# Kernel tuning notes

Hardware: AMD Instinct MI355X
Metric: run time of the kernel (lower is better)

Reference implementation:

```python
import jax, jax.numpy as jnp
import numpy as np

N_A = 50000
N_B = 50000
E = 500000
D = 128


def setup_inputs() -> dict:
    key = jax.random.key(0)
    ks = jax.random.split(key, 16)
    s = 0.02
    inp = {
        "x_a": jax.random.normal(ks[0], (N_A, D), jnp.float32),
        "x_b": jax.random.normal(ks[1], (N_B, D), jnp.float32),
        # shared GraphEdgeWeight params
        "Wp": jax.random.normal(ks[2], (D, D), jnp.float32) * s,
        "bp": jnp.zeros((D,), jnp.float32),
        "Wc": jax.random.normal(ks[3], (D, D), jnp.float32) * s,
        "bc": jnp.zeros((D,), jnp.float32),
        "W1": jax.random.normal(ks[4], (D, 3 * D), jnp.float32) * s,
        "b1": jnp.zeros((D,), jnp.float32),
        "W2": jax.random.normal(ks[5], (1, D), jnp.float32) * s,
        "b2": jnp.zeros((1,), jnp.float32),
        # GraphConv params for edge type A->B
        "Wrel_ab": jax.random.normal(ks[6], (D, D), jnp.float32) * s,
        "brel_ab": jnp.zeros((D,), jnp.float32),
        "Wroot_ab": jax.random.normal(ks[7], (D, D), jnp.float32) * s,
        "broot_ab": jnp.zeros((D,), jnp.float32),
        # GraphConv params for edge type B->A
        "Wrel_ba": jax.random.normal(ks[8], (D, D), jnp.float32) * s,
        "brel_ba": jnp.zeros((D,), jnp.float32),
        "Wroot_ba": jax.random.normal(ks[9], (D, D), jnp.float32) * s,
        "broot_ba": jnp.zeros((D,), jnp.float32),
        # edge indices: row0 = src node ids, row1 = dst node ids
        "ei_ab": jax.random.randint(ks[10], (2, E), 0, N_A),
        "ei_ba": jax.random.randint(ks[11], (2, E), 0, N_B),
    }
    return inp


def _edge_type_conv(x_src, x_dst, ei, Wp, bp, Wc, bc, W1, b1, W2, b2,
                    Wrel, brel, Wroot, broot, n_dst):
    # gather endpoint features per edge  [E, D]
    par = x_src[ei[0]]
    cld = x_dst[ei[1]]
    # GraphEdgeWeight: encoders (Linear + LeakyReLU; dropout inactive in eval)
    ep = jax.nn.leaky_relu(par @ Wp.T + bp, negative_slope=0.01)
    ec = jax.nn.leaky_relu(cld @ Wc.T + bc, negative_slope=0.01)
    feat = jnp.concatenate([ep, ec, jnp.abs(par - cld)], axis=-1)  # [E, 3D]
    h = jax.nn.relu(feat @ W1.T + b1)                              # [E, D]
    w = jax.nn.sigmoid(h @ W2.T + b2)[:, 0]                        # [E]
    # GraphConv: out_i = Wrel @ sum_{j->i} w_e x_j + Wroot @ x_i (+ biases)
    msg = jax.ops.segment_sum(par * w[:, None], ei[1], num_segments=n_dst)
    return msg @ Wrel.T + brel + x_dst @ Wroot.T + broot


def reference(x_a, x_b, Wp, bp, Wc, bc, W1, b1, W2, b2,
              Wrel_ab, brel_ab, Wroot_ab, broot_ab,
              Wrel_ba, brel_ba, Wroot_ba, broot_ba,
              ei_ab, ei_ba):
    out_b = _edge_type_conv(x_a, x_b, ei_ab, Wp, bp, Wc, bc, W1, b1, W2, b2,
                            Wrel_ab, brel_ab, Wroot_ab, broot_ab, N_B)
    out_a = _edge_type_conv(x_b, x_a, ei_ba, Wp, bp, Wc, bc, W1, b1, W2, b2,
                            Wrel_ba, brel_ba, Wroot_ba, broot_ba, N_A)
    return out_a, out_b
```

## Files before the change

kernel.cpp:

```cpp
#include <hip/hip_runtime.h>
#include <hip/hip_bf16.h>

typedef unsigned short u16;
typedef __attribute__((ext_vector_type(8))) short bf16x8;
typedef __attribute__((ext_vector_type(2))) short s16x2;
typedef __attribute__((ext_vector_type(4))) float f32x4;

#define N_NODES 50000
#define EDGES 500000
#define WPT 31250
#define NWAVES 3125
#define NBLK 782

__device__ __forceinline__ u16 f2bf(float f) {
  return __builtin_bit_cast(u16, __float2bfloat16(f));
}
__device__ __forceinline__ float bf2f(u16 u) {
  return __builtin_bit_cast(float, ((unsigned)u) << 16);
}
__device__ __forceinline__ float bfe(bf16x8 v, int j) {
  return bf2f((u16)v[j]);
}

__device__ __forceinline__ void pk_atomic_bf16(u16* addr, float lo, float hi) {
#if __has_builtin(__builtin_amdgcn_global_atomic_fadd_v2bf16)
  s16x2 v;
  v[0] = (short)f2bf(lo);
  v[1] = (short)f2bf(hi);
  __builtin_amdgcn_global_atomic_fadd_v2bf16(
      (__attribute__((address_space(1))) s16x2*)addr, v);
#else
  unsigned* p = (unsigned*)addr;
  unsigned old = *p, assumed;
  do {
    assumed = old;
    float l2 = bf2f((u16)(assumed & 0xffff)) + lo;
    float h2 = bf2f((u16)(assumed >> 16)) + hi;
    unsigned nv = (unsigned)f2bf(l2) | ((unsigned)f2bf(h2) << 16);
    old = atomicCAS(p, assumed, nv);
  } while (old != assumed);
#endif
}

__global__ __launch_bounds__(256) void prep_weights(
    const float* __restrict__ Wp, const float* __restrict__ Wc,
    const float* __restrict__ W1,
    const float* __restrict__ Wrel_ab, const float* __restrict__ Wroot_ab,
    const float* __restrict__ Wrel_ba, const float* __restrict__ Wroot_ba,
    u16* __restrict__ out)
{
  int tid = blockIdx.x * 256 + threadIdx.x;
  int m = tid >> 14;
  int idx = tid & 16383;
  int r = idx >> 7;
  int c = idx & 127;
  float val;
  switch (m) {
    case 0: val = Wp[r * 128 + c]; break;
    case 1: val = Wc[r * 128 + c]; break;
    case 2: val = W1[r * 384 + c]; break;
    case 3: val = W1[r * 384 + 128 + c]; break;
    case 4: val = W1[r * 384 + 256 + c]; break;
    case 5: val = Wrel_ab[r * 128 + c]; break;
    case 6: val = Wroot_ab[r * 128 + c]; break;
    case 7: val = Wrel_ba[r * 128 + c]; break;
    default: val = Wroot_ba[r * 128 + c]; break;
  }
  out[tid] = f2bf(val);
}

__global__ __launch_bounds__(256) void cast_x(
    const float* __restrict__ xa, const float* __restrict__ xb,
    u16* __restrict__ oa, u16* __restrict__ ob)
{
  int t = blockIdx.x * 256 + threadIdx.x;
  const int HALF = (N_NODES * 128) / 8;
  const float* src;
  u16* dst;
  int idx;
  if (t < HALF) { src = xa; dst = oa; idx = t * 8; }
  else          { src = xb; dst = ob; idx = (t - HALF) * 8; }
  f32x4 a = *(const f32x4*)(src + idx);
  f32x4 b = *(const f32x4*)(src + idx + 4);
  bf16x8 o;
#pragma unroll
  for (int j = 0; j < 4; j++) {
    o[j]     = (short)f2bf(a[j]);
    o[j + 4] = (short)f2bf(b[j]);
  }
  *(bf16x8*)(dst + idx) = o;
}

__global__ __launch_bounds__(256) void encoder2(
    const u16* __restrict__ xa_bf, const u16* __restrict__ xb_bf,
    const u16* __restrict__ Wp_b, const float* __restrict__ bp,
    const u16* __restrict__ Wc_b, const float* __restrict__ bc,
    const u16* __restrict__ W1a_b, const float* __restrict__ b1,
    const u16* __restrict__ W1b_b,
    u16* __restrict__ u_a, u16* __restrict__ v_a,
    u16* __restrict__ u_b, u16* __restrict__ v_b)
{
  __shared__ u16 tile[4][2176];
  int widx = threadIdx.x >> 6;
  int w = blockIdx.x * 4 + widx;
  int type = (w >= NBLK * 4) ? 1 : 0;
  int nw = w - type * NBLK * 4;
  if (nw >= NWAVES) nw = NWAVES - 1;
  const u16* xbf = type ? xb_bf : xa_bf;
  u16* u_out = type ? u_b : u_a;
  u16* v_out = type ? v_b : v_a;
  int row0 = nw * 16;
  int lane = threadIdx.x & 63;
  int col = lane & 15;
  int quad = lane >> 4;
  u16* tl = tile[widx];

  bf16x8 af[4];
#pragma unroll
  for (int ks = 0; ks < 4; ks++)
    af[ks] = *(const bf16x8*)(xbf + (size_t)(row0 + col) * 128 + ks * 32 + quad * 8);

  f32x4 zero = {0.f, 0.f, 0.f, 0.f};

  for (int chain = 0; chain < 2; chain++) {
    const u16* Wenc = chain ? Wc_b : Wp_b;
    const float* benc = chain ? bc : bp;
    const u16* Wmix = chain ? W1b_b : W1a_b;
    const float* bmix = chain ? nullptr : b1;
    u16* outp = chain ? v_out : u_out;

    f32x4 acc[8];
#pragma unroll
    for (int nt = 0; nt < 8; nt++) acc[nt] = zero;
#pragma unroll
    for (int ks = 0; ks < 4; ks++) {
      const u16* wp = Wenc + col * 128 + ks * 32 + quad * 8;
#pragma unroll
      for (int nt = 0; nt < 8; nt++) {
        bf16x8 bf = *(const bf16x8*)(wp + nt * 2048);
        acc[nt] = __builtin_amdgcn_mfma_f32_16x16x32_bf16(af[ks], bf, acc[nt], 0, 0, 0);
      }
    }
#pragma unroll
    for (int nt = 0; nt < 8; nt++) {
      float be = benc[nt * 16 + col];
#pragma unroll
      for (int r = 0; r < 4; r++) {
        float v = acc[nt][r] + be;
        v = v > 0.f ? v : 0.01f * v;
        tl[(quad * 4 + r) * 136 + nt * 16 + col] = f2bf(v);
      }
    }
    bf16x8 a2[4];
#pragma unroll
    for (int ks = 0; ks < 4; ks++)
      a2[ks] = *(const bf16x8*)&tl[col * 136 + ks * 32 + quad * 8];

    f32x4 acc2[8];
#pragma unroll
    for (int nt = 0; nt < 8; nt++) acc2[nt] = zero;
#pragma unroll
    for (int ks = 0; ks < 4; ks++) {
      const u16* wp = Wmix + col * 128 + ks * 32 + quad * 8;
#pragma unroll
      for (int nt = 0; nt < 8; nt++) {
        bf16x8 bf = *(const bf16x8*)(wp + nt * 2048);
        acc2[nt] = __builtin_amdgcn_mfma_f32_16x16x32_bf16(a2[ks], bf, acc2[nt], 0, 0, 0);
      }
    }
#pragma unroll
    for (int nt = 0; nt < 8; nt++) {
      float bm = bmix ? bmix[nt * 16 + col] : 0.f;
#pragma unroll
      for (int r = 0; r < 4; r++)
        outp[(size_t)(row0 + quad * 4 + r) * 128 + nt * 16 + col] = f2bf(acc2[nt][r] + bm);
    }
  }
}

__global__ __launch_bounds__(256) void out_gemm2(
    const u16* __restrict__ xa_bf, const u16* __restrict__ xb_bf,
    const u16* __restrict__ msgX_a, const u16* __restrict__ msgX_b,
    const u16* __restrict__ Wrelba_b, const u16* __restrict__ Wrelab_b,
    const u16* __restrict__ Wrootba_b, const u16* __restrict__ Wrootab_b,
    const float* __restrict__ brel_ba, const float* __restrict__ broot_ba,
    const float* __restrict__ brel_ab, const float* __restrict__ broot_ab,
    float* __restrict__ out_a, float* __restrict__ out_b)
{
  int w = blockIdx.x * 4 + (threadIdx.x >> 6);
  int type = (w >= NBLK * 4) ? 1 : 0;
  int nw = w - type * NBLK * 4;
  if (nw >= NWAVES) return;
  const u16* xbf = type ? xb_bf : xa_bf;
  const u16* msg = type ? msgX_b : msgX_a;
  const u16* Wrel = type ? Wrelab_b : Wrelba_b;
  const u16* Wroot = type ? Wrootab_b : Wrootba_b;
  const float* brel = type ? brel_ab : brel_ba;
  const float* broot = type ? broot_ab : broot_ba;
  float* outp = type ? out_b : out_a;
  int row0 = nw * 16;
  int lane = threadIdx.x & 63;
  int col = lane & 15;
  int quad = lane >> 4;

  bf16x8 ax[4], am[4];
#pragma unroll
  for (int ks = 0; ks < 4; ks++) {
    ax[ks] = *(const bf16x8*)(xbf + (size_t)(row0 + col) * 128 + ks * 32 + quad * 8);
    am[ks] = *(const bf16x8*)(msg + (size_t)(row0 + col) * 128 + ks * 32 + quad * 8);
  }

  f32x4 zero = {0.f, 0.f, 0.f, 0.f};
  f32x4 acc[8];
#pragma unroll
  for (int nt = 0; nt < 8; nt++) acc[nt] = zero;
#pragma unroll
  for (int ks = 0; ks < 4; ks++) {
    const u16* wp1 = Wrel + col * 128 + ks * 32 + quad * 8;
    const u16* wp2 = Wroot + col * 128 + ks * 32 + quad * 8;
#pragma unroll
    for (int nt = 0; nt < 8; nt++) {
      bf16x8 b1f = *(const bf16x8*)(wp1 + nt * 2048);
      acc[nt] = __builtin_amdgcn_mfma_f32_16x16x32_bf16(am[ks], b1f, acc[nt], 0, 0, 0);
      bf16x8 b2f = *(const bf16x8*)(wp2 + nt * 2048);
      acc[nt] = __builtin_amdgcn_mfma_f32_16x16x32_bf16(ax[ks], b2f, acc[nt], 0, 0, 0);
    }
  }
#pragma unroll
  for (int nt = 0; nt < 8; nt++) {
    int c = nt * 16 + col;
    float b = brel[c] + broot[c];
#pragma unroll
    for (int r = 0; r < 4; r++)
      outp[(size_t)(row0 + quad * 4 + r) * 128 + c] = acc[nt][r] + b;
  }
}

__global__ __launch_bounds__(256) void edge_fused(
    const u16* __restrict__ xa_bf, const u16* __restrict__ xb_bf,
    const int* __restrict__ ei_ab, const int* __restrict__ ei_ba,
    const u16* __restrict__ W1c,
    const u16* __restrict__ u_a, const u16* __restrict__ v_a,
    const u16* __restrict__ u_b, const u16* __restrict__ v_b,
    const float* __restrict__ W2, const float* __restrict__ b2p,
    u16* __restrict__ msgX_a, u16* __restrict__ msgX_b)
{
  __shared__ u16 tld[4][2176];
  int widx = threadIdx.x >> 6;
  int w = blockIdx.x * 4 + widx;
  int type = (w >= WPT) ? 1 : 0;
  int e0 = (w - type * WPT) * 16;
  const u16* xs = type ? xb_bf : xa_bf;
  const u16* xd = type ? xa_bf : xb_bf;
  const int* ei = type ? ei_ba : ei_ab;
  const u16* uT = type ? u_b : u_a;
  const u16* vT = type ? v_a : v_b;
  u16* msgX     = type ? msgX_a : msgX_b;

  int lane = threadIdx.x & 63;
  int col = lane & 15;
  int quad = lane >> 4;

  int em = e0 + col;
  int si = ei[em];
  int di = ei[EDGES + em];

  bf16x8 af[4];
  bf16x8 df[4];
#pragma unroll
  for (int ks = 0; ks < 4; ks++) {
    af[ks] = *(const bf16x8*)(xs + (size_t)si * 128 + ks * 32 + quad * 8);
    bf16x8 d8 = *(const bf16x8*)(xd + (size_t)di * 128 + ks * 32 + quad * 8);
#pragma unroll
    for (int j = 0; j < 8; j++)
      df[ks][j] = (short)f2bf(__builtin_fabsf(bfe(af[ks], j) - bfe(d8, j)));
  }

  f32x4 zero = {0.f, 0.f, 0.f, 0.f};
  f32x4 acc[8];
#pragma unroll
  for (int nt = 0; nt < 8; nt++) acc[nt] = zero;
#pragma unroll
  for (int ks = 0; ks < 4; ks++) {
    const u16* wp = W1c + col * 128 + ks * 32 + quad * 8;
#pragma unroll
    for (int nt = 0; nt < 8; nt++) {
      bf16x8 bf = *(const bf16x8*)(wp + nt * 2048);
      acc[nt] = __builtin_amdgcn_mfma_f32_16x16x32_bf16(df[ks], bf, acc[nt], 0, 0, 0);
    }
  }

  u16* tl = tld[widx];
#pragma unroll
  for (int nt = 0; nt < 8; nt++)
#pragma unroll
    for (int r = 0; r < 4; r++)
      tl[(quad * 4 + r) * 136 + nt * 16 + col] = f2bf(acc[nt][r]);

  int e = e0 + (lane >> 2);
  int s2 = ei[e];
  int d2 = ei[EDGES + e];
  int c0 = (lane & 3) * 32;
  const u16* trow = &tl[(lane >> 2) * 136 + c0];
  const u16* urow = uT + (size_t)s2 * 128 + c0;
  const u16* vrow = vT + (size_t)d2 * 128 + c0;

  float p = 0.f;
#pragma unroll
  for (int k = 0; k < 4; k++) {
    bf16x8 tt = *(const bf16x8*)(trow + k * 8);
    bf16x8 uu = *(const bf16x8*)(urow + k * 8);
    bf16x8 vv = *(const bf16x8*)(vrow + k * 8);
    f32x4 w0 = *(const f32x4*)(W2 + c0 + k * 8);
    f32x4 w1 = *(const f32x4*)(W2 + c0 + k * 8 + 4);
#pragma unroll
    for (int j = 0; j < 4; j++) {
      float q0 = bfe(tt, j) + bfe(uu, j) + bfe(vv, j);
      if (q0 > 0.f) p += q0 * w0[j];
      float q1 = bfe(tt, j + 4) + bfe(uu, j + 4) + bfe(vv, j + 4);
      if (q1 > 0.f) p += q1 * w1[j];
    }
  }
  p += __shfl_xor(p, 1, 64);
  p += __shfl_xor(p, 2, 64);
  float wgt = 1.f / (1.f + __expf(-(p + b2p[0])));

#pragma unroll
  for (int ks = 0; ks < 4; ks++)
    *(bf16x8*)&tl[col * 136 + ks * 32 + quad * 8] = af[ks];

#pragma unroll
  for (int r = 0; r < 4; r++) {
    int src_lane = (quad * 4 + r) * 4;
    float wr = __shfl(wgt, src_lane, 64);
    int dr = __shfl(d2, src_lane, 64);
    u16* mrow = msgX + (size_t)dr * 128;
    const u16* xrow = &tl[(quad * 4 + r) * 136];
#pragma unroll
    for (int nt = 0; nt < 4; nt++) {
      int c = nt * 32 + col * 2;
      unsigned xv = *(const unsigned*)(xrow + c);
      pk_atomic_bf16(mrow + c, wr * bf2f((u16)(xv & 0xffff)),
                               wr * bf2f((u16)(xv >> 16)));
    }
  }
}

extern "C" void kernel_launch(void* const* d_in, const int* in_sizes, int n_in,
                              void* d_out, int out_size, void* d_ws, size_t ws_size,
                              hipStream_t stream) {
  const float* x_a      = (const float*)d_in[0];
  const float* x_b      = (const float*)d_in[1];
  const float* Wp       = (const float*)d_in[2];
  const float* bp       = (const float*)d_in[3];
  const float* Wc       = (const float*)d_in[4];
  const float* bc       = (const float*)d_in[5];
  const float* W1       = (const float*)d_in[6];
  const float* b1       = (const float*)d_in[7];
  const float* W2       = (const float*)d_in[8];
  const float* b2       = (const float*)d_in[9];
  const float* Wrel_ab  = (const float*)d_in[10];
  const float* brel_ab  = (const float*)d_in[11];
  const float* Wroot_ab = (const float*)d_in[12];
  const float* broot_ab = (const float*)d_in[13];
  const float* Wrel_ba  = (const float*)d_in[14];
  const float* brel_ba  = (const float*)d_in[15];
  const float* Wroot_ba = (const float*)d_in[16];
  const float* broot_ba = (const float*)d_in[17];
  const int*   ei_ab    = (const int*)d_in[18];
  const int*   ei_ba    = (const int*)d_in[19];

  char* ws = (char*)d_ws;
  u16* Wb        = (u16*)ws;
  u16* Wp_b      = Wb + 0 * 16384;
  u16* Wc_b      = Wb + 1 * 16384;
  u16* W1a_b     = Wb + 2 * 16384;
  u16* W1b_b     = Wb + 3 * 16384;
  u16* W1c_b     = Wb + 4 * 16384;
  u16* Wrelab_b  = Wb + 5 * 16384;
  u16* Wrootab_b = Wb + 6 * 16384;
  u16* Wrelba_b  = Wb + 7 * 16384;
  u16* Wrootba_b = Wb + 8 * 16384;

  u16* xa_bf   = (u16*)(ws + 1048576);
  u16* xb_bf   = (u16*)(ws + 13848576);
  u16* u_a     = (u16*)(ws + 26648576);
  u16* v_a     = (u16*)(ws + 39448576);
  u16* u_b     = (u16*)(ws + 52248576);
  u16* v_b     = (u16*)(ws + 65048576);
  u16* msgX_a  = (u16*)(ws + 77848576);
  u16* msgX_b  = (u16*)(ws + 90648576);

  float* out_a = (float*)d_out;
  float* out_b = out_a + (size_t)N_NODES * 128;

  hipMemsetAsync(msgX_a, 0, (size_t)2 * N_NODES * 128 * sizeof(u16), stream);

  prep_weights<<<576, 256, 0, stream>>>(Wp, Wc, W1, Wrel_ab, Wroot_ab,
                                        Wrel_ba, Wroot_ba, Wb);
  cast_x<<<6250, 256, 0, stream>>>(x_a, x_b, xa_bf, xb_bf);

  encoder2<<<2 * NBLK, 256, 0, stream>>>(xa_bf, xb_bf, Wp_b, bp, Wc_b, bc,
                                         W1a_b, b1, W1b_b, u_a, v_a, u_b, v_b);

  edge_fused<<<15625, 256, 0, stream>>>(xa_bf, xb_bf, ei_ab, ei_ba, W1c_b,
                                        u_a, v_a, u_b, v_b,
                                        W2, b2, msgX_a, msgX_b);

  out_gemm2<<<2 * NBLK, 256, 0, stream>>>(xa_bf, xb_bf, msgX_a, msgX_b,
                                          Wrelba_b, Wrelab_b,
                                          Wrootba_b, Wrootab_b,
                                          brel_ba, broot_ba, brel_ab, broot_ab,
                                          out_a, out_b);
}
```

Measured before the change: 698.0 us.

## Make the edge kernel persistent with prefetch, and fold the cast and memset into other kernels

The edge kernel becomes persistent with a grid-stride loop over 16-edge groups. Each iteration issues the next group's index and endpoint-feature gathers while the current group's MFMA, scoring and atomic scatter run, so gather latency is hidden. The occupancy hint in launch bounds is raised. The fp32-to-bf16 cast of x is folded into the encoder kernel, and zeroing of the message buffers is folded into the weight-prep kernel, which removes a cast launch and a memset. In exchange, the prefetched fragments raise register pressure, and the fixed grid of 2048 blocks may leave load imbalance across CUs.

```diff
diff --git a/kernel.cpp b/kernel.cpp
--- a/kernel.cpp
+++ b/kernel.cpp
@@ -9,6 +9,9 @@
 #define N_NODES 50000
 #define EDGES 500000
 #define WPT 31250
+#define EG_TOTAL 62500
+#define EG_BLOCKS 2048
+#define EG_WAVES (EG_BLOCKS * 4)
 #define NWAVES 3125
 #define NBLK 782
 
@@ -42,13 +45,19 @@
 #endif
 }
 
-__global__ __launch_bounds__(256) void prep_weights(
+__global__ __launch_bounds__(256) void prep_weights_zero(
     const float* __restrict__ Wp, const float* __restrict__ Wc,
     const float* __restrict__ W1,
     const float* __restrict__ Wrel_ab, const float* __restrict__ Wroot_ab,
     const float* __restrict__ Wrel_ba, const float* __restrict__ Wroot_ba,
-    u16* __restrict__ out)
+    u16* __restrict__ out, u16* __restrict__ msg)
 {
+  if (blockIdx.x >= 576) {
+    size_t t = (size_t)(blockIdx.x - 576) * 256 + threadIdx.x;
+    bf16x8 z = {0, 0, 0, 0, 0, 0, 0, 0};
+    *(bf16x8*)(msg + t * 8) = z;
+    return;
+  }
   int tid = blockIdx.x * 256 + threadIdx.x;
   int m = tid >> 14;
   int idx = tid & 16383;
@@ -69,34 +78,13 @@
   out[tid] = f2bf(val);
 }
 
-__global__ __launch_bounds__(256) void cast_x(
+__global__ __launch_bounds__(256) void encoder2(
     const float* __restrict__ xa, const float* __restrict__ xb,
-    u16* __restrict__ oa, u16* __restrict__ ob)
-{
-  int t = blockIdx.x * 256 + threadIdx.x;
-  const int HALF = (N_NODES * 128) / 8;
-  const float* src;
-  u16* dst;
-  int idx;
-  if (t < HALF) { src = xa; dst = oa; idx = t * 8; }
-  else          { src = xb; dst = ob; idx = (t - HALF) * 8; }
-  f32x4 a = *(const f32x4*)(src + idx);
-  f32x4 b = *(const f32x4*)(src + idx + 4);
-  bf16x8 o;
-#pragma unroll
-  for (int j = 0; j < 4; j++) {
-    o[j]     = (short)f2bf(a[j]);
-    o[j + 4] = (short)f2bf(b[j]);
-  }
-  *(bf16x8*)(dst + idx) = o;
-}
-
-__global__ __launch_bounds__(256) void encoder2(
-    const u16* __restrict__ xa_bf, const u16* __restrict__ xb_bf,
     const u16* __restrict__ Wp_b, const float* __restrict__ bp,
     const u16* __restrict__ Wc_b, const float* __restrict__ bc,
     const u16* __restrict__ W1a_b, const float* __restrict__ b1,
     const u16* __restrict__ W1b_b,
+    u16* __restrict__ xa_bf, u16* __restrict__ xb_bf,
     u16* __restrict__ u_a, u16* __restrict__ v_a,
     u16* __restrict__ u_b, u16* __restrict__ v_b)
 {
@@ -106,7 +94,8 @@
   int type = (w >= NBLK * 4) ? 1 : 0;
   int nw = w - type * NBLK * 4;
   if (nw >= NWAVES) nw = NWAVES - 1;
-  const u16* xbf = type ? xb_bf : xa_bf;
+  const float* x = type ? xb : xa;
+  u16* xbf_out = type ? xb_bf : xa_bf;
   u16* u_out = type ? u_b : u_a;
   u16* v_out = type ? v_b : v_a;
   int row0 = nw * 16;
@@ -117,8 +106,19 @@
 
   bf16x8 af[4];
 #pragma unroll
-  for (int ks = 0; ks < 4; ks++)
-    af[ks] = *(const bf16x8*)(xbf + (size_t)(row0 + col) * 128 + ks * 32 + quad * 8);
+  for (int ks = 0; ks < 4; ks++) {
+    const float* xp = x + (size_t)(row0 + col) * 128 + ks * 32 + quad * 8;
+    f32x4 lo = *(const f32x4*)xp;
+    f32x4 hi = *(const f32x4*)(xp + 4);
+    bf16x8 o;
+#pragma unroll
+    for (int j = 0; j < 4; j++) {
+      o[j]     = (short)f2bf(lo[j]);
+      o[j + 4] = (short)f2bf(hi[j]);
+    }
+    af[ks] = o;
+    *(bf16x8*)(xbf_out + (size_t)(row0 + col) * 128 + ks * 32 + quad * 8) = o;
+  }
 
   f32x4 zero = {0.f, 0.f, 0.f, 0.f};
 
@@ -236,7 +236,7 @@
   }
 }
 
-__global__ __launch_bounds__(256) void edge_fused(
+__global__ __launch_bounds__(256, 3) void edge_fused(
     const u16* __restrict__ xa_bf, const u16* __restrict__ xb_bf,
     const int* __restrict__ ei_ab, const int* __restrict__ ei_ba,
     const u16* __restrict__ W1c,
@@ -246,102 +246,143 @@
     u16* __restrict__ msgX_a, u16* __restrict__ msgX_b)
 {
   __shared__ u16 tld[4][2176];
-  int widx = threadIdx.x >> 6;
-  int w = blockIdx.x * 4 + widx;
-  int type = (w >= WPT) ? 1 : 0;
-  int e0 = (w - type * WPT) * 16;
-  const u16* xs = type ? xb_bf : xa_bf;
-  const u16* xd = type ? xa_bf : xb_bf;
-  const int* ei = type ? ei_ba : ei_ab;
-  const u16* uT = type ? u_b : u_a;
-  const u16* vT = type ? v_a : v_b;
-  u16* msgX     = type ? msgX_a : msgX_b;
-
-  int lane = threadIdx.x & 63;
-  int col = lane & 15;
-  int quad = lane >> 4;
-
-  int em = e0 + col;
-  int si = ei[em];
-  int di = ei[EDGES + em];
-
-  bf16x8 af[4];
-  bf16x8 df[4];
-#pragma unroll
-  for (int ks = 0; ks < 4; ks++) {
-    af[ks] = *(const bf16x8*)(xs + (size_t)si * 128 + ks * 32 + quad * 8);
-    bf16x8 d8 = *(const bf16x8*)(xd + (size_t)di * 128 + ks * 32 + quad * 8);
-#pragma unroll
-    for (int j = 0; j < 8; j++)
-      df[ks][j] = (short)f2bf(__builtin_fabsf(bfe(af[ks], j) - bfe(d8, j)));
-  }
-
-  f32x4 zero = {0.f, 0.f, 0.f, 0.f};
-  f32x4 acc[8];
-#pragma unroll
-  for (int nt = 0; nt < 8; nt++) acc[nt] = zero;
-#pragma unroll
-  for (int ks = 0; ks < 4; ks++) {
-    const u16* wp = W1c + col * 128 + ks * 32 + quad * 8;
-#pragma unroll
-    for (int nt = 0; nt < 8; nt++) {
-      bf16x8 bf = *(const bf16x8*)(wp + nt * 2048);
-      acc[nt] = __builtin_amdgcn_mfma_f32_16x16x32_bf16(df[ks], bf, acc[nt], 0, 0, 0);
-    }
-  }
-
+  const int widx = threadIdx.x >> 6;
+  const int lane = threadIdx.x & 63;
+  const int col = lane & 15;
+  const int quad = lane >> 4;
+  const int e4 = lane >> 2;
+  const int c0 = (lane & 3) * 32;
   u16* tl = tld[widx];
-#pragma unroll
-  for (int nt = 0; nt < 8; nt++)
-#pragma unroll
-    for (int r = 0; r < 4; r++)
-      tl[(quad * 4 + r) * 136 + nt * 16 + col] = f2bf(acc[nt][r]);
-
-  int e = e0 + (lane >> 2);
-  int s2 = ei[e];
-  int d2 = ei[EDGES + e];
-  int c0 = (lane & 3) * 32;
-  const u16* trow = &tl[(lane >> 2) * 136 + c0];
-  const u16* urow = uT + (size_t)s2 * 128 + c0;
-  const u16* vrow = vT + (size_t)d2 * 128 + c0;
-
-  float p = 0.f;
-#pragma unroll
-  for (int k = 0; k < 4; k++) {
-    bf16x8 tt = *(const bf16x8*)(trow + k * 8);
-    bf16x8 uu = *(const bf16x8*)(urow + k * 8);
-    bf16x8 vv = *(const bf16x8*)(vrow + k * 8);
-    f32x4 w0 = *(const f32x4*)(W2 + c0 + k * 8);
-    f32x4 w1 = *(const f32x4*)(W2 + c0 + k * 8 + 4);
-#pragma unroll
-    for (int j = 0; j < 4; j++) {
-      float q0 = bfe(tt, j) + bfe(uu, j) + bfe(vv, j);
-      if (q0 > 0.f) p += q0 * w0[j];
-      float q1 = bfe(tt, j + 4) + bfe(uu, j + 4) + bfe(vv, j + 4);
-      if (q1 > 0.f) p += q1 * w1[j];
-    }
-  }
-  p += __shfl_xor(p, 1, 64);
-  p += __shfl_xor(p, 2, 64);
-  float wgt = 1.f / (1.f + __expf(-(p + b2p[0])));
-
-#pragma unroll
-  for (int ks = 0; ks < 4; ks++)
-    *(bf16x8*)&tl[col * 136 + ks * 32 + quad * 8] = af[ks];
-
-#pragma unroll
-  for (int r = 0; r < 4; r++) {
-    int src_lane = (quad * 4 + r) * 4;
-    float wr = __shfl(wgt, src_lane, 64);
-    int dr = __shfl(d2, src_lane, 64);
-    u16* mrow = msgX + (size_t)dr * 128;
-    const u16* xrow = &tl[(quad * 4 + r) * 136];
-#pragma unroll
-    for (int nt = 0; nt < 4; nt++) {
-      int c = nt * 32 + col * 2;
-      unsigned xv = *(const unsigned*)(xrow + c);
-      pk_atomic_bf16(mrow + c, wr * bf2f((u16)(xv & 0xffff)),
-                               wr * bf2f((u16)(xv >> 16)));
+
+  const int gid0 = blockIdx.x * 4 + widx;
+
+  int s2, d2;
+  bf16x8 AF[4], BD[4];
+  {
+    int t0 = (gid0 >= WPT) ? 1 : 0;
+    const int* ei = t0 ? ei_ba : ei_ab;
+    int e0 = (gid0 - t0 * WPT) * 16;
+    int si = ei[e0 + col];
+    int di = ei[EDGES + e0 + col];
+    s2 = ei[e0 + e4];
+    d2 = ei[EDGES + e0 + e4];
+    const u16* xs = t0 ? xb_bf : xa_bf;
+    const u16* xd = t0 ? xa_bf : xb_bf;
+#pragma unroll
+    for (int ks = 0; ks < 4; ks++) {
+      AF[ks] = *(const bf16x8*)(xs + (size_t)si * 128 + ks * 32 + quad * 8);
+      BD[ks] = *(const bf16x8*)(xd + (size_t)di * 128 + ks * 32 + quad * 8);
+    }
+  }
+
+  for (int g = gid0; g < EG_TOTAL; g += EG_WAVES) {
+    int ty = (g >= WPT) ? 1 : 0;
+    const u16* uT = ty ? u_b : u_a;
+    const u16* vT = ty ? v_a : v_b;
+    u16* msgX = ty ? msgX_a : msgX_b;
+
+    const u16* urow = uT + (size_t)s2 * 128 + c0;
+    const u16* vrow = vT + (size_t)d2 * 128 + c0;
+    bf16x8 UU[4], VV[4];
+#pragma unroll
+    for (int k = 0; k < 4; k++) {
+      UU[k] = *(const bf16x8*)(urow + k * 8);
+      VV[k] = *(const bf16x8*)(vrow + k * 8);
+    }
+
+    int gn = g + EG_WAVES;
+    bool hasn = gn < EG_TOTAL;
+    int sin = 0, din = 0, s2n = 0, d2n = 0;
+    const u16* xsn = xa_bf;
+    const u16* xdn = xa_bf;
+    if (hasn) {
+      int tn = (gn >= WPT) ? 1 : 0;
+      const int* ein = tn ? ei_ba : ei_ab;
+      int e0n = (gn - tn * WPT) * 16;
+      sin = ein[e0n + col];
+      din = ein[EDGES + e0n + col];
+      s2n = ein[e0n + e4];
+      d2n = ein[EDGES + e0n + e4];
+      xsn = tn ? xb_bf : xa_bf;
+      xdn = tn ? xa_bf : xb_bf;
+    }
+
+    f32x4 zero = {0.f, 0.f, 0.f, 0.f};
+    f32x4 acc[8];
+#pragma unroll
+    for (int nt = 0; nt < 8; nt++) acc[nt] = zero;
+#pragma unroll
+    for (int ks = 0; ks < 4; ks++) {
+      bf16x8 df;
+#pragma unroll
+      for (int j = 0; j < 8; j++)
+        df[j] = (short)f2bf(__builtin_fabsf(bfe(AF[ks], j) - bfe(BD[ks], j)));
+      const u16* wp = W1c + col * 128 + ks * 32 + quad * 8;
+#pragma unroll
+      for (int nt = 0; nt < 8; nt++) {
+        bf16x8 bf = *(const bf16x8*)(wp + nt * 2048);
+        acc[nt] = __builtin_amdgcn_mfma_f32_16x16x32_bf16(df, bf, acc[nt], 0, 0, 0);
+      }
+    }
+
+    bf16x8 AFn[4], BDn[4];
+    if (hasn) {
+#pragma unroll
+      for (int ks = 0; ks < 4; ks++) {
+        AFn[ks] = *(const bf16x8*)(xsn + (size_t)sin * 128 + ks * 32 + quad * 8);
+        BDn[ks] = *(const bf16x8*)(xdn + (size_t)din * 128 + ks * 32 + quad * 8);
+      }
+    }
+
+#pragma unroll
+    for (int nt = 0; nt < 8; nt++)
+#pragma unroll
+      for (int r = 0; r < 4; r++)
+        tl[(quad * 4 + r) * 136 + nt * 16 + col] = f2bf(acc[nt][r]);
+
+    const u16* trow = &tl[e4 * 136 + c0];
+    float p = 0.f;
+#pragma unroll
+    for (int k = 0; k < 4; k++) {
+      bf16x8 tt = *(const bf16x8*)(trow + k * 8);
+      f32x4 w0 = *(const f32x4*)(W2 + c0 + k * 8);
+      f32x4 w1 = *(const f32x4*)(W2 + c0 + k * 8 + 4);
+#pragma unroll
+      for (int j = 0; j < 4; j++) {
+        float q0 = bfe(tt, j) + bfe(UU[k], j) + bfe(VV[k], j);
+        if (q0 > 0.f) p += q0 * w0[j];
+        float q1 = bfe(tt, j + 4) + bfe(UU[k], j + 4) + bfe(VV[k], j + 4);
+        if (q1 > 0.f) p += q1 * w1[j];
+      }
+    }
+    p += __shfl_xor(p, 1, 64);
+    p += __shfl_xor(p, 2, 64);
+    float wgt = 1.f / (1.f + __expf(-(p + b2p[0])));
+
+#pragma unroll
+    for (int ks = 0; ks < 4; ks++)
+      *(bf16x8*)&tl[col * 136 + ks * 32 + quad * 8] = AF[ks];
+#pragma unroll
+    for (int r = 0; r < 4; r++) {
+      int src_lane = (quad * 4 + r) * 4;
+      float wr = __shfl(wgt, src_lane, 64);
+      int dr = __shfl(d2, src_lane, 64);
+      u16* mrow = msgX + (size_t)dr * 128;
+      const u16* xrow = &tl[(quad * 4 + r) * 136];
+#pragma unroll
+      for (int nt = 0; nt < 4; nt++) {
+        int c = nt * 32 + col * 2;
+        unsigned xv = *(const unsigned*)(xrow + c);
+        pk_atomic_bf16(mrow + c, wr * bf2f((u16)(xv & 0xffff)),
+                                 wr * bf2f((u16)(xv >> 16)));
+      }
+    }
+
+    if (hasn) {
+#pragma unroll
+      for (int ks = 0; ks < 4; ks++) { AF[ks] = AFn[ks]; BD[ks] = BDn[ks]; }
+      s2 = s2n;
+      d2 = d2n;
     }
   }
 }
@@ -394,18 +435,16 @@
   float* out_a = (float*)d_out;
   float* out_b = out_a + (size_t)N_NODES * 128;
 
-  hipMemsetAsync(msgX_a, 0, (size_t)2 * N_NODES * 128 * sizeof(u16), stream);
-
-  prep_weights<<<576, 256, 0, stream>>>(Wp, Wc, W1, Wrel_ab, Wroot_ab,
-                                        Wrel_ba, Wroot_ba, Wb);
-  cast_x<<<6250, 256, 0, stream>>>(x_a, x_b, xa_bf, xb_bf);
-
-  encoder2<<<2 * NBLK, 256, 0, stream>>>(xa_bf, xb_bf, Wp_b, bp, Wc_b, bc,
-                                         W1a_b, b1, W1b_b, u_a, v_a, u_b, v_b);
-
-  edge_fused<<<15625, 256, 0, stream>>>(xa_bf, xb_bf, ei_ab, ei_ba, W1c_b,
-                                        u_a, v_a, u_b, v_b,
-                                        W2, b2, msgX_a, msgX_b);
+  prep_weights_zero<<<6826, 256, 0, stream>>>(Wp, Wc, W1, Wrel_ab, Wroot_ab,
+                                              Wrel_ba, Wroot_ba, Wb, msgX_a);
+
+  encoder2<<<2 * NBLK, 256, 0, stream>>>(x_a, x_b, Wp_b, bp, Wc_b, bc,
+                                         W1a_b, b1, W1b_b,
+                                         xa_bf, xb_bf, u_a, v_a, u_b, v_b);
+
+  edge_fused<<<EG_BLOCKS, 256, 0, stream>>>(xa_bf, xb_bf, ei_ab, ei_ba, W1c_b,
+                                            u_a, v_a, u_b, v_b,
+                                            W2, b2, msgX_a, msgX_b);
 
   out_gemm2<<<2 * NBLK, 256, 0, stream>>>(xa_bf, xb_bf, msgX_a, msgX_b,
                                           Wrelba_b, Wrelab_b,
```

New measurement: 947.6 us. +35.8%, slower.

## Fuse x casting into encoder, memset into weight prep, hoist edge loads

Applied to the files above, without the earlier changes.

The separate cast_x kernel is removed. The encoder now reads fp32 node features, converts them to bf16 in registers for its MFMA inputs, and writes the bf16 copy for later kernels to use. The hipMemsetAsync of the message buffers moves into extra blocks of the weight-prep kernel, cutting launch count and one full read of x. In edge_fused, the u/v gathers are issued before the MFMA chain, and the abs-diff conversion moves into the k-loop, to overlap gather latency with compute at the cost of more live registers.

```diff
diff --git a/kernel.cpp b/kernel.cpp
--- a/kernel.cpp
+++ b/kernel.cpp
@@ -42,13 +42,19 @@
 #endif
 }
 
-__global__ __launch_bounds__(256) void prep_weights(
+__global__ __launch_bounds__(256) void prep_weights_zero(
     const float* __restrict__ Wp, const float* __restrict__ Wc,
     const float* __restrict__ W1,
     const float* __restrict__ Wrel_ab, const float* __restrict__ Wroot_ab,
     const float* __restrict__ Wrel_ba, const float* __restrict__ Wroot_ba,
-    u16* __restrict__ out)
+    u16* __restrict__ out, u16* __restrict__ msg)
 {
+  if (blockIdx.x >= 576) {
+    size_t t = (size_t)(blockIdx.x - 576) * 256 + threadIdx.x;
+    bf16x8 z = {0, 0, 0, 0, 0, 0, 0, 0};
+    *(bf16x8*)(msg + t * 8) = z;
+    return;
+  }
   int tid = blockIdx.x * 256 + threadIdx.x;
   int m = tid >> 14;
   int idx = tid & 16383;
@@ -69,34 +75,13 @@
   out[tid] = f2bf(val);
 }
 
-__global__ __launch_bounds__(256) void cast_x(
+__global__ __launch_bounds__(256) void encoder2(
     const float* __restrict__ xa, const float* __restrict__ xb,
-    u16* __restrict__ oa, u16* __restrict__ ob)
-{
-  int t = blockIdx.x * 256 + threadIdx.x;
-  const int HALF = (N_NODES * 128) / 8;
-  const float* src;
-  u16* dst;
-  int idx;
-  if (t < HALF) { src = xa; dst = oa; idx = t * 8; }
-  else          { src = xb; dst = ob; idx = (t - HALF) * 8; }
-  f32x4 a = *(const f32x4*)(src + idx);
-  f32x4 b = *(const f32x4*)(src + idx + 4);
-  bf16x8 o;
-#pragma unroll
-  for (int j = 0; j < 4; j++) {
-    o[j]     = (short)f2bf(a[j]);
-    o[j + 4] = (short)f2bf(b[j]);
-  }
-  *(bf16x8*)(dst + idx) = o;
-}
-
-__global__ __launch_bounds__(256) void encoder2(
-    const u16* __restrict__ xa_bf, const u16* __restrict__ xb_bf,
     const u16* __restrict__ Wp_b, const float* __restrict__ bp,
     const u16* __restrict__ Wc_b, const float* __restrict__ bc,
     const u16* __restrict__ W1a_b, const float* __restrict__ b1,
     const u16* __restrict__ W1b_b,
+    u16* __restrict__ xa_bf, u16* __restrict__ xb_bf,
     u16* __restrict__ u_a, u16* __restrict__ v_a,
     u16* __restrict__ u_b, u16* __restrict__ v_b)
 {
@@ -106,7 +91,8 @@
   int type = (w >= NBLK * 4) ? 1 : 0;
   int nw = w - type * NBLK * 4;
   if (nw >= NWAVES) nw = NWAVES - 1;
-  const u16* xbf = type ? xb_bf : xa_bf;
+  const float* x = type ? xb : xa;
+  u16* xbf_out = type ? xb_bf : xa_bf;
   u16* u_out = type ? u_b : u_a;
   u16* v_out = type ? v_b : v_a;
   int row0 = nw * 16;
@@ -117,8 +103,19 @@
 
   bf16x8 af[4];
 #pragma unroll
-  for (int ks = 0; ks < 4; ks++)
-    af[ks] = *(const bf16x8*)(xbf + (size_t)(row0 + col) * 128 + ks * 32 + quad * 8);
+  for (int ks = 0; ks < 4; ks++) {
+    const float* xp = x + (size_t)(row0 + col) * 128 + ks * 32 + quad * 8;
+    f32x4 lo = *(const f32x4*)xp;
+    f32x4 hi = *(const f32x4*)(xp + 4);
+    bf16x8 o;
+#pragma unroll
+    for (int j = 0; j < 4; j++) {
+      o[j]     = (short)f2bf(lo[j]);
+      o[j + 4] = (short)f2bf(hi[j]);
+    }
+    af[ks] = o;
+    *(bf16x8*)(xbf_out + (size_t)(row0 + col) * 128 + ks * 32 + quad * 8) = o;
+  }
 
   f32x4 zero = {0.f, 0.f, 0.f, 0.f};
 
@@ -265,59 +262,65 @@
   int si = ei[em];
   int di = ei[EDGES + em];
 
-  bf16x8 af[4];
-  bf16x8 df[4];
-#pragma unroll
-  for (int ks = 0; ks < 4; ks++) {
-    af[ks] = *(const bf16x8*)(xs + (size_t)si * 128 + ks * 32 + quad * 8);
-    bf16x8 d8 = *(const bf16x8*)(xd + (size_t)di * 128 + ks * 32 + quad * 8);
-#pragma unroll
-    for (int j = 0; j < 8; j++)
-      df[ks][j] = (short)f2bf(__builtin_fabsf(bfe(af[ks], j) - bfe(d8, j)));
-  }
-
-  f32x4 zero = {0.f, 0.f, 0.f, 0.f};
-  f32x4 acc[8];
-#pragma unroll
-  for (int nt = 0; nt < 8; nt++) acc[nt] = zero;
-#pragma unroll
-  for (int ks = 0; ks < 4; ks++) {
-    const u16* wp = W1c + col * 128 + ks * 32 + quad * 8;
-#pragma unroll
-    for (int nt = 0; nt < 8; nt++) {
-      bf16x8 bf = *(const bf16x8*)(wp + nt * 2048);
-      acc[nt] = __builtin_amdgcn_mfma_f32_16x16x32_bf16(df[ks], bf, acc[nt], 0, 0, 0);
-    }
-  }
-
-  u16* tl = tld[widx];
-#pragma unroll
-  for (int nt = 0; nt < 8; nt++)
-#pragma unroll
-    for (int r = 0; r < 4; r++)
-      tl[(quad * 4 + r) * 136 + nt * 16 + col] = f2bf(acc[nt][r]);
-
   int e = e0 + (lane >> 2);
   int s2 = ei[e];
   int d2 = ei[EDGES + e];
   int c0 = (lane & 3) * 32;
-  const u16* trow = &tl[(lane >> 2) * 136 + c0];
+
+  bf16x8 af[4];
+  bf16x8 d8[4];
+#pragma unroll
+  for (int ks = 0; ks < 4; ks++) {
+    af[ks] = *(const bf16x8*)(xs + (size_t)si * 128 + ks * 32 + quad * 8);
+    d8[ks] = *(const bf16x8*)(xd + (size_t)di * 128 + ks * 32 + quad * 8);
+  }
+
   const u16* urow = uT + (size_t)s2 * 128 + c0;
   const u16* vrow = vT + (size_t)d2 * 128 + c0;
-
+  bf16x8 UU[4], VV[4];
+#pragma unroll
+  for (int k = 0; k < 4; k++) {
+    UU[k] = *(const bf16x8*)(urow + k * 8);
+    VV[k] = *(const bf16x8*)(vrow + k * 8);
+  }
+
+  f32x4 zero = {0.f, 0.f, 0.f, 0.f};
+  f32x4 acc[8];
+#pragma unroll
+  for (int nt = 0; nt < 8; nt++) acc[nt] = zero;
+#pragma unroll
+  for (int ks = 0; ks < 4; ks++) {
+    bf16x8 df;
+#pragma unroll
+    for (int j = 0; j < 8; j++)
+      df[j] = (short)f2bf(__builtin_fabsf(bfe(af[ks], j) - bfe(d8[ks], j)));
+    const u16* wp = W1c + col * 128 + ks * 32 + quad * 8;
+#pragma unroll
+    for (int nt = 0; nt < 8; nt++) {
+      bf16x8 bf = *(const bf16x8*)(wp + nt * 2048);
+      acc[nt] = __builtin_amdgcn_mfma_f32_16x16x32_bf16(df, bf, acc[nt], 0, 0, 0);
+    }
+  }
+
+  u16* tl = tld[widx];
+#pragma unroll
+  for (int nt = 0; nt < 8; nt++)
+#pragma unroll
+    for (int r = 0; r < 4; r++)
+      tl[(quad * 4 + r) * 136 + nt * 16 + col] = f2bf(acc[nt][r]);
+
+  const u16* trow = &tl[(lane >> 2) * 136 + c0];
   float p = 0.f;
 #pragma unroll
   for (int k = 0; k < 4; k++) {
     bf16x8 tt = *(const bf16x8*)(trow + k * 8);
-    bf16x8 uu = *(const bf16x8*)(urow + k * 8);
-    bf16x8 vv = *(const bf16x8*)(vrow + k * 8);
     f32x4 w0 = *(const f32x4*)(W2 + c0 + k * 8);
     f32x4 w1 = *(const f32x4*)(W2 + c0 + k * 8 + 4);
 #pragma unroll
     for (int j = 0; j < 4; j++) {
-      float q0 = bfe(tt, j) + bfe(uu, j) + bfe(vv, j);
+      float q0 = bfe(tt, j) + bfe(UU[k], j) + bfe(VV[k], j);
       if (q0 > 0.f) p += q0 * w0[j];
-      float q1 = bfe(tt, j + 4) + bfe(uu, j + 4) + bfe(vv, j + 4);
+      float q1 = bfe(tt, j + 4) + bfe(UU[k], j + 4) + bfe(VV[k], j + 4);
       if (q1 > 0.f) p += q1 * w1[j];
     }
   }
@@ -394,14 +397,12 @@
   float* out_a = (float*)d_out;
   float* out_b = out_a + (size_t)N_NODES * 128;
 
-  hipMemsetAsync(msgX_a, 0, (size_t)2 * N_NODES * 128 * sizeof(u16), stream);
-
-  prep_weights<<<576, 256, 0, stream>>>(Wp, Wc, W1, Wrel_ab, Wroot_ab,
-                                        Wrel_ba, Wroot_ba, Wb);
-  cast_x<<<6250, 256, 0, stream>>>(x_a, x_b, xa_bf, xb_bf);
-
-  encoder2<<<2 * NBLK, 256, 0, stream>>>(xa_bf, xb_bf, Wp_b, bp, Wc_b, bc,
-                                         W1a_b, b1, W1b_b, u_a, v_a, u_b, v_b);
+  prep_weights_zero<<<6826, 256, 0, stream>>>(Wp, Wc, W1, Wrel_ab, Wroot_ab,
+                                              Wrel_ba, Wroot_ba, Wb, msgX_a);
+
+  encoder2<<<2 * NBLK, 256, 0, stream>>>(x_a, x_b, Wp_b, bp, Wc_b, bc,
+                                         W1a_b, b1, W1b_b,
+                                         xa_bf, xb_bf, u_a, v_a, u_b, v_b);
 
   edge_fused<<<15625, 256, 0, stream>>>(xa_bf, xb_bf, ei_ab, ei_ba, W1c_b,
                                         u_a, v_a, u_b, v_b,
```

Result: no change. 697.9 us (-0.0%).
